# Kernel tuning notes

Hardware: AMD Instinct MI355X
Metric: run time of the kernel (lower is better)

The kernel has to match this reference:

```python
import jax, jax.numpy as jnp
import numpy as np

EPS = 1e-06

def setup_inputs() -> dict:
    key = jax.random.key(0)
    kx, kq, kk, kv = jax.random.split(key, 4)
    B, S, D, F = 8, 4096, 1024, 1024
    # glorot-uniform-ish scale for weights
    scale = (6.0 / (D + F)) ** 0.5
    x = jax.random.normal(kx, (B, S, D), dtype=jnp.float32)
    Wq = jax.random.uniform(kq, (D, F), dtype=jnp.float32, minval=-scale, maxval=scale)
    Wk = jax.random.uniform(kk, (D, F), dtype=jnp.float32, minval=-scale, maxval=scale)
    Wv = jax.random.uniform(kv, (D, F), dtype=jnp.float32, minval=-scale, maxval=scale)
    return {"x": x, "Wq": Wq, "Wk": Wk, "Wv": Wv}


def reference(x, Wq, Wk, Wv):
    # x: [B, S, D]; projections -> [B, S, F]
    queries = jnp.einsum('bsd,df->bsf', x, Wq)
    keys = jnp.einsum('bsd,df->bsf', x, Wk)
    values = jnp.einsum('bsd,df->bsf', x, Wv)
    # feature map: relu(.) + 1 (strictly positive kernel features)
    queries = jax.nn.relu(queries) + 1.0
    keys = jax.nn.relu(keys) + 1.0
    # numerator: K^T V over sequence -> [B, F, F]
    numerator = jnp.einsum('bsf,bsg->bfg', keys, values)
    # denominator: sum of keys over sequence -> [B, 1, F]; broadcasts over last axis
    denominator = jnp.sum(keys, axis=-2, keepdims=True)
    context = numerator / (denominator + EPS)
    # output: context @ Q^T -> [B, F, S]
    output = jnp.einsum('bfg,bsg->bfs', context, queries)
    return output
```

## Files before the change

### kernel.cpp

```cpp
#include <hip/hip_runtime.h>


#define EPSF 1e-6f

constexpr int Bb = 8;
constexpr int Ss = 4096;
constexpr int Dd = 1024;
constexpr int Ff = 1024;

typedef __attribute__((ext_vector_type(8))) short   bf16x8;
typedef __attribute__((ext_vector_type(8))) unsigned short u16x8;
typedef __attribute__((ext_vector_type(4))) float   f32x4;

typedef __attribute__((address_space(3))) unsigned char lds_u8;
typedef __attribute__((address_space(3))) const bf16x8  lds_cvec;

static __device__ __forceinline__ unsigned short f2bf(float f) {
    union { float f; unsigned int u; } v; v.f = f;
    unsigned int r = (v.u + 0x7fffu + ((v.u >> 16) & 1u)) >> 16;
    return (unsigned short)r;
}
static __device__ __forceinline__ float bf2f(unsigned short u) {
    union { unsigned int u; float f; } v; v.u = ((unsigned int)u) << 16;
    return v.f;
}

static __device__ __forceinline__ void gld_lds16(const void* g, lds_u8* l) {
    __builtin_amdgcn_global_load_lds(
        (const __attribute__((address_space(1))) unsigned int*)g,
        (__attribute__((address_space(3))) unsigned int*)l,
        16, 0, 0);
}

__global__ void cvt_x_kernel(const float* __restrict__ x, unsigned short* __restrict__ xb, int n4)
{
    int i = blockIdx.x * blockDim.x + threadIdx.x;
    if (i >= n4) return;
    float4 v = *(const float4*)&x[(size_t)i * 4];
    ushort4 o;
    o.x = f2bf(v.x); o.y = f2bf(v.y); o.z = f2bf(v.z); o.w = f2bf(v.w);
    *(ushort4*)&xb[(size_t)i * 4] = o;
}

__global__ void cvt_wT_kernel(const float* __restrict__ Wq,
                              const float* __restrict__ Wk,
                              const float* __restrict__ Wv,
                              unsigned short* __restrict__ WT)
{
    const int z = blockIdx.z;
    const float* __restrict__ W = (z == 0) ? Wq : (z == 1 ? Wk : Wv);
    unsigned short* __restrict__ dst = WT + (size_t)z * Dd * Ff;

    __shared__ float tile[32][33];
    const int tid = threadIdx.x;
    const int d0 = blockIdx.y * 32, f0 = blockIdx.x * 32;
    const int c = tid & 31, r8 = tid >> 5;
#pragma unroll
    for (int p = 0; p < 4; ++p) {
        int r = p * 8 + r8;
        tile[r][c] = W[(size_t)(d0 + r) * Ff + f0 + c];
    }
    __syncthreads();
#pragma unroll
    for (int p = 0; p < 4; ++p) {
        int r = p * 8 + r8;
        dst[(size_t)(f0 + r) * Dd + d0 + c] = f2bf(tile[c][r]);
    }
}

__global__ void den_kernel(const unsigned short* __restrict__ KbT, float* __restrict__ den)
{
    const int tid = threadIdx.x;
    const int w = tid >> 6, lane = tid & 63;
    const int f = blockIdx.x * 4 + w;
    const int b = blockIdx.y;
    const unsigned short* __restrict__ row = KbT + ((size_t)b * Ff + f) * Ss;
    float s = 0.f;
#pragma unroll
    for (int it = 0; it < Ss / 512; ++it) {
        u16x8 v = *(const u16x8*)&row[it * 512 + lane * 8];
#pragma unroll
        for (int j = 0; j < 8; ++j) s += bf2f(v[j]);
    }
#pragma unroll
    for (int off = 32; off > 0; off >>= 1) s += __shfl_down(s, off, 64);
    if (lane == 0) den[(size_t)b * Ff + f] = s;
}

__global__ void add_ctx_kernel(const unsigned short* __restrict__ p,
                               unsigned short* __restrict__ c)
{
    const int b = blockIdx.y;
    const size_t i8 = ((size_t)blockIdx.x * 256 + threadIdx.x) * 8;
    const u16x8 a0 = *(const u16x8*)(p + (size_t)(2 * b) * Ff * Ff + i8);
    const u16x8 a1 = *(const u16x8*)(p + (size_t)(2 * b + 1) * Ff * Ff + i8);
    u16x8 o;
#pragma unroll
    for (int j = 0; j < 8; ++j) o[j] = f2bf(bf2f(a0[j]) + bf2f(a1[j]));
    *(u16x8*)(c + (size_t)b * Ff * Ff + i8) = o;
}

template<int ACT, int SCALE, int OUT_BF16, int SPLITK2>
__global__ __launch_bounds__(256, 2)
void gemm8(const unsigned short* __restrict__ A,
           const unsigned short* __restrict__ Bt,
           void* __restrict__ Cout,
           const float* __restrict__ den,
           int lda, int ldb, int ldc, int Kdim,
           size_t strideA, size_t strideB, size_t strideC)
{
    __shared__ __align__(16) unsigned char smem_[65536];
    lds_u8* const smem = (lds_u8*)smem_;

    const int gx = gridDim.x, gxy = gx * gridDim.y;
    int flat = blockIdx.z * gxy + blockIdx.y * gx + blockIdx.x;
    const int nwg = gxy * gridDim.z;
    const int cpx = nwg >> 3;
    flat = (flat & 7) * cpx + (flat >> 3);
    const int z = flat / gxy;
    const int rem = flat - z * gxy;
    const int by = rem / gx;
    const int bx = rem - by * gx;

    const int zb   = SPLITK2 ? (z >> 1) : z;
    const int koff = SPLITK2 ? ((z & 1) * Kdim) : 0;

    const unsigned short* __restrict__ Ag  = A  + strideA * zb + koff;
    const unsigned short* __restrict__ Bg  = Bt + strideB * zb + koff;
    const float* __restrict__ denb = SCALE ? (den + (size_t)zb * Ff) : nullptr;

    const int bm = by * 128;
    const int bn = bx * 128;

    const int tid  = threadIdx.x;
    const int wv   = tid >> 6, lane = tid & 63;
    const int wm   = wv >> 1, wn = wv & 1;
    const int lm   = lane & 15;
    const int kg16 = (lane >> 4) << 4;
    const int swz  = (lm & 7) << 4;
    const int kbs  = (((tid & 7) ^ ((tid >> 3) & 7)) << 4);
    const int srow = tid >> 3;

    f32x4 acc[4][4];
#pragma unroll
    for (int i = 0; i < 4; ++i)
#pragma unroll
        for (int j = 0; j < 4; ++j) acc[i][j] = (f32x4){0.f, 0.f, 0.f, 0.f};

    auto STAGE = [&](int ts, int m, int buf) {
        const unsigned short* gb = m ? Bg : Ag;
        const int ld = m ? ldb : lda;
        const int off0 = m ? bn : bm;
        lds_u8* lb = smem + buf * 32768 + m * 16384 + wv * 1024;
#pragma unroll
        for (int q = 0; q < 4; ++q) {
            int row = q * 32 + srow;
            const unsigned char* g =
                (const unsigned char*)(gb + (size_t)(off0 + row) * ld + ts * 64) + kbs;
            gld_lds16(g, lb + q * 4096);
        }
    };
    auto LD4 = [&](bf16x8* dst, int kk, lds_u8* base, int w0) {
#pragma unroll
        for (int f = 0; f < 4; ++f) {
            int r = w0 * 64 + f * 16 + lm;
            dst[f] = *(lds_cvec*)(base + r * 128 + ((kk * 64 + kg16) ^ swz));
        }
    };

#define MM16(a4, b4)                                                            \
    do {                                                                        \
        __builtin_amdgcn_s_setprio(1);                                          \
        _Pragma("unroll")                                                       \
        for (int fm = 0; fm < 4; ++fm)                                          \
            _Pragma("unroll")                                                   \
            for (int fn = 0; fn < 4; ++fn)                                      \
                acc[fm][fn] = __builtin_amdgcn_mfma_f32_16x16x32_bf16(          \
                    (b4)[fn], (a4)[fm], acc[fm][fn], 0, 0, 0);                  \
        __builtin_amdgcn_s_setprio(0);                                          \
    } while (0)

#define LGKM0_FENCE()                                               \
    do {                                                            \
        asm volatile("s_waitcnt lgkmcnt(0)");                       \
        __builtin_amdgcn_sched_barrier(0);                          \
    } while (0)

    const int NT = Kdim >> 6;

    STAGE(0, 0, 0); STAGE(0, 1, 0);
    asm volatile("s_waitcnt vmcnt(0)");
    __builtin_amdgcn_s_barrier();

    for (int t = 0; t < NT; ++t) {
        const int buf = t & 1;
        lds_u8* Ab  = smem + buf * 32768;
        lds_u8* Bbs = Ab + 16384;
        if (t + 1 < NT) {
            STAGE(t + 1, 0, buf ^ 1);
            STAGE(t + 1, 1, buf ^ 1);
        }
        bf16x8 a0[4], b0r[4], a1[4], b1r[4];
        LD4(a0, 0, Ab, wm); LD4(b0r, 0, Bbs, wn);
        LGKM0_FENCE();
        MM16(a0, b0r);
        LD4(a1, 1, Ab, wm); LD4(b1r, 1, Bbs, wn);
        LGKM0_FENCE();
        MM16(a1, b1r);
        asm volatile("s_waitcnt vmcnt(0)");
        __builtin_amdgcn_sched_barrier(0);
        __builtin_amdgcn_s_barrier();
    }

    const int hi4 = (lane >> 4) * 4;
#pragma unroll
    for (int fm = 0; fm < 4; ++fm) {
        const int gr = bm + wm * 64 + fm * 16 + lm;
#pragma unroll
        for (int fn = 0; fn < 4; ++fn) {
            const int gcn = bn + wn * 64 + fn * 16 + hi4;
            f32x4 v = acc[fm][fn];
            if (ACT) {
#pragma unroll
                for (int e = 0; e < 4; ++e) v[e] = fmaxf(v[e], 0.f) + 1.f;
            }
            if (SCALE) {
                float4 d4 = *(const float4*)&denb[gcn];
                v[0] *= 1.f / (d4.x + EPSF);
                v[1] *= 1.f / (d4.y + EPSF);
                v[2] *= 1.f / (d4.z + EPSF);
                v[3] *= 1.f / (d4.w + EPSF);
            }
            if (OUT_BF16) {
                ushort4 o;
                o.x = f2bf(v[0]); o.y = f2bf(v[1]); o.z = f2bf(v[2]); o.w = f2bf(v[3]);
                *(ushort4*)((unsigned short*)Cout + strideC * z + (size_t)gr * ldc + gcn) = o;
            } else {
                *(float4*)((float*)Cout + strideC * z + (size_t)gr * ldc + gcn) =
                    *(float4*)&v;
            }
        }
    }
#undef MM16
#undef LGKM0_FENCE
}

extern "C" void kernel_launch(void* const* d_in, const int* in_sizes, int n_in,
                              void* d_out, int out_size, void* d_ws, size_t ws_size,
                              hipStream_t stream)
{
    (void)in_sizes; (void)n_in; (void)out_size;
    const float* x  = (const float*)d_in[0];
    const float* Wq = (const float*)d_in[1];
    const float* Wk = (const float*)d_in[2];
    const float* Wv = (const float*)d_in[3];
    float* out = (float*)d_out;

    const size_t nx   = (size_t)Bb * Ss * Dd;
    const size_t nW   = (size_t)3 * Dd * Ff;
    const size_t nQKV = (size_t)Bb * Ss * Ff;
    const size_t nCtx = (size_t)Bb * Ff * Ff;
    const size_t nP   = (size_t)16 * Ff * Ff;

    unsigned short* xb   = (unsigned short*)d_ws;
    unsigned short* WT   = xb + nx;
    unsigned short* Qb   = WT + nW;
    unsigned short* KbT  = Qb + nQKV;
    unsigned short* VbT  = KbT + nQKV;
    unsigned short* ctxb = VbT + nQKV;
    float* den = (float*)(ctxb + nCtx);
    unsigned short* pctx = (unsigned short*)(den + (size_t)Bb * Ff);

    const size_t need_split =
        ((nx + nW + 3 * nQKV + nCtx + nP) * 2 + (size_t)Bb * Ff * 4);
    const bool do_split = ws_size >= need_split;

    cvt_x_kernel<<<dim3((int)(nx / 4 / 256)), 256, 0, stream>>>(x, xb, (int)(nx / 4));
    cvt_wT_kernel<<<dim3(Ff / 32, Dd / 32, 3), 256, 0, stream>>>(Wq, Wk, Wv, WT);

    gemm8<1, 0, 1, 0><<<dim3(Ss / 128, Ff / 128, Bb), 256, 0, stream>>>(
        WT + (size_t)1 * Dd * Ff, xb, KbT, nullptr,
        Dd, Dd, Ss, Dd, 0, (size_t)Ss * Dd, (size_t)Ff * Ss);

    den_kernel<<<dim3(Ff / 4, Bb), 256, 0, stream>>>(KbT, den);

    gemm8<1, 1, 1, 0><<<dim3(Ff / 128, Ss / 128, Bb), 256, 0, stream>>>(
        xb, WT + (size_t)0 * Dd * Ff, Qb, den,
        Dd, Dd, Ff, Dd, (size_t)Ss * Dd, 0, (size_t)Ss * Ff);

    gemm8<0, 0, 1, 0><<<dim3(Ss / 128, Ff / 128, Bb), 256, 0, stream>>>(
        WT + (size_t)2 * Dd * Ff, xb, VbT, nullptr,
        Dd, Dd, Ss, Dd, 0, (size_t)Ss * Dd, (size_t)Ff * Ss);

    if (do_split) {
        gemm8<0, 0, 1, 1><<<dim3(Ff / 128, Ff / 128, 2 * Bb), 256, 0, stream>>>(
            KbT, VbT, pctx, nullptr,
            Ss, Ss, Ff, Ss / 2, (size_t)Ff * Ss, (size_t)Ff * Ss, (size_t)Ff * Ff);
        add_ctx_kernel<<<dim3(Ff * Ff / 8 / 256, Bb), 256, 0, stream>>>(pctx, ctxb);
    } else {
        gemm8<0, 0, 1, 0><<<dim3(Ff / 128, Ff / 128, Bb), 256, 0, stream>>>(
            KbT, VbT, ctxb, nullptr,
            Ss, Ss, Ff, Ss, (size_t)Ff * Ss, (size_t)Ff * Ss, (size_t)Ff * Ff);
    }

    gemm8<0, 0, 0, 0><<<dim3(Ss / 128, Ff / 128, Bb), 256, 0, stream>>>(
        ctxb, Qb, out, nullptr,
        Ff, Ff, Ss, Ff, (size_t)Ff * Ff, (size_t)Ss * Ff, (size_t)Ff * Ss);
}
```

Measured before the change: 480.5 us.

## Replace double-buffered GEMM staging with single buffer and raise occupancy

The GEMM main loop drops its LDS double buffer and prefetch of the next K tile. Each iteration now loads the current tile into a single 32 KB buffer, syncs, computes, and syncs again. Halving LDS use and raising the launch-bounds waves hint to 3 aims to fit more workgroups per CU and hide latency through occupancy instead of software pipelining. Manual waitcnt fences and MFMA priority hints are removed and left to the compiler, which gives up explicit overlap of global loads with MFMA work.

```diff
diff --git a/kernel.cpp b/kernel.cpp
--- a/kernel.cpp
+++ b/kernel.cpp
@@ -101,7 +101,7 @@
 }
 
 template<int ACT, int SCALE, int OUT_BF16, int SPLITK2>
-__global__ __launch_bounds__(256, 2)
+__global__ __launch_bounds__(256, 3)
 void gemm8(const unsigned short* __restrict__ A,
            const unsigned short* __restrict__ Bt,
            void* __restrict__ Cout,
@@ -109,7 +109,7 @@
            int lda, int ldb, int ldc, int Kdim,
            size_t strideA, size_t strideB, size_t strideC)
 {
-    __shared__ __align__(16) unsigned char smem_[65536];
+    __shared__ __align__(16) unsigned char smem_[32768];
     lds_u8* const smem = (lds_u8*)smem_;
 
     const int gx = gridDim.x, gxy = gx * gridDim.y;
@@ -147,11 +147,14 @@
 #pragma unroll
         for (int j = 0; j < 4; ++j) acc[i][j] = (f32x4){0.f, 0.f, 0.f, 0.f};
 
-    auto STAGE = [&](int ts, int m, int buf) {
+    lds_u8* const Ab  = smem;
+    lds_u8* const Bbs = smem + 16384;
+
+    auto STAGE = [&](int ts, int m) {
         const unsigned short* gb = m ? Bg : Ag;
         const int ld = m ? ldb : lda;
         const int off0 = m ? bn : bm;
-        lds_u8* lb = smem + buf * 32768 + m * 16384 + wv * 1024;
+        lds_u8* lb = smem + m * 16384 + wv * 1024;
 #pragma unroll
         for (int q = 0; q < 4; ++q) {
             int row = q * 32 + srow;
@@ -170,46 +173,26 @@
 
 #define MM16(a4, b4)                                                            \
     do {                                                                        \
-        __builtin_amdgcn_s_setprio(1);                                          \
         _Pragma("unroll")                                                       \
         for (int fm = 0; fm < 4; ++fm)                                          \
             _Pragma("unroll")                                                   \
             for (int fn = 0; fn < 4; ++fn)                                      \
                 acc[fm][fn] = __builtin_amdgcn_mfma_f32_16x16x32_bf16(          \
                     (b4)[fn], (a4)[fm], acc[fm][fn], 0, 0, 0);                  \
-        __builtin_amdgcn_s_setprio(0);                                          \
     } while (0)
 
-#define LGKM0_FENCE()                                               \
-    do {                                                            \
-        asm volatile("s_waitcnt lgkmcnt(0)");                       \
-        __builtin_amdgcn_sched_barrier(0);                          \
-    } while (0)
-
     const int NT = Kdim >> 6;
 
-    STAGE(0, 0, 0); STAGE(0, 1, 0);
-    asm volatile("s_waitcnt vmcnt(0)");
-    __builtin_amdgcn_s_barrier();
-
     for (int t = 0; t < NT; ++t) {
-        const int buf = t & 1;
-        lds_u8* Ab  = smem + buf * 32768;
-        lds_u8* Bbs = Ab + 16384;
-        if (t + 1 < NT) {
-            STAGE(t + 1, 0, buf ^ 1);
-            STAGE(t + 1, 1, buf ^ 1);
-        }
+        STAGE(t, 0);
+        STAGE(t, 1);
+        __syncthreads();
         bf16x8 a0[4], b0r[4], a1[4], b1r[4];
         LD4(a0, 0, Ab, wm); LD4(b0r, 0, Bbs, wn);
-        LGKM0_FENCE();
         MM16(a0, b0r);
         LD4(a1, 1, Ab, wm); LD4(b1r, 1, Bbs, wn);
-        LGKM0_FENCE();
         MM16(a1, b1r);
-        asm volatile("s_waitcnt vmcnt(0)");
-        __builtin_amdgcn_sched_barrier(0);
-        __builtin_amdgcn_s_barrier();
+        __syncthreads();
     }
 
     const int hi4 = (lane >> 4) * 4;
@@ -242,7 +225,6 @@
         }
     }
 #undef MM16
-#undef LGKM0_FENCE
 }
 
 extern "C" void kernel_launch(void* const* d_in, const int* in_sizes, int n_in,
```

Measured after the change: 442.2 us. -8.0%, faster.
